# Optimization experiments

Measured on AMD Instinct MI355X. Metric: run time of the kernel, lower is better.

## Reference

```python
import jax, jax.numpy as jnp
import numpy as np

N_NODES = 50000
N_EDGES = 1600000
N_FEAT = 50
HID = 20
OUT_DIM = 10
N_GRAPHS = 64


def _glorot(key, shape):
    fan_in, fan_out = shape[0], shape[1]
    lim = float(np.sqrt(6.0 / (fan_in + fan_out)))
    return jax.random.uniform(key, shape, jnp.float32, -lim, lim)


def setup_inputs() -> dict:
    key = jax.random.key(0)
    ks = jax.random.split(key, 16)
    x = jax.random.normal(ks[0], (N_NODES, N_FEAT), jnp.float32)
    edge_index = jax.random.randint(ks[1], (2, N_EDGES), 0, N_NODES, jnp.int32)
    batch = jnp.sort(jax.random.randint(ks[2], (N_NODES,), 0, N_GRAPHS, jnp.int32))
    inp = {"x": x, "edge_index": edge_index, "batch": batch}
    # GraphConv layer params: lin_rel (weight+bias, applied to aggregated msgs), lin_root (no bias)
    dims = [(N_FEAT, HID), (HID, HID), (HID, HID)]
    for i, (di, do) in enumerate(dims, start=1):
        inp[f"W_rel{i}"] = _glorot(ks[3 * i], (di, do))
        inp[f"W_root{i}"] = _glorot(ks[3 * i + 1], (di, do))
        inp[f"b{i}"] = jnp.zeros((do,), jnp.float32)
    # final Linear on cat([max_pool, mean_pool]) -> in_features = 2*HID
    inp["W_lin"] = _glorot(ks[13], (2 * HID, OUT_DIM))
    inp["b_lin"] = jnp.zeros((OUT_DIM,), jnp.float32)
    return inp


def _graph_conv(x, src, dst, W_rel, W_root, b):
    # PyG GraphConv: aggregate raw neighbor features (sum), then linear.
    agg = jax.ops.segment_sum(x[src], dst, num_segments=N_NODES)  # [N, d_in]
    return agg @ W_rel + x @ W_root + b


def reference(x, edge_index, batch,
              W_rel1, W_root1, b1,
              W_rel2, W_root2, b2,
              W_rel3, W_root3, b3,
              W_lin, b_lin):
    src, dst = edge_index[0], edge_index[1]
    h = jax.nn.relu(_graph_conv(x, src, dst, W_rel1, W_root1, b1))
    h = jax.nn.relu(_graph_conv(h, src, dst, W_rel2, W_root2, b2))
    h = jax.nn.relu(_graph_conv(h, src, dst, W_rel3, W_root3, b3))
    # global max / mean pool per graph
    maxP = jax.ops.segment_max(h, batch, num_segments=N_GRAPHS)  # [G, HID]
    sums = jax.ops.segment_sum(h, batch, num_segments=N_GRAPHS)
    cnt = jax.ops.segment_sum(jnp.ones((h.shape[0], 1), h.dtype), batch, num_segments=N_GRAPHS)
    meanP = sums / jnp.maximum(cnt, 1.0)
    return jnp.concatenate([maxP, meanP], axis=-1) @ W_lin + b_lin
```

## Files before the change

### kernel.cpp

```cpp
#include <hip/hip_runtime.h>

#define N_NODES  50000
#define N_EDGES  1600000
#define N_FEAT   50
#define HID      20
#define OUT_DIM  10
#define N_GRAPHS 64

#define NBUCK 196
#define BCAP  10240
#define EPB   (N_EDGES/256)
#define G50B  977


__global__ __launch_bounds__(1024) void k1_gemm_scatter(
        const float* __restrict__ x, const float* __restrict__ Wrel,
        const float* __restrict__ Wroot, const float* __restrict__ b,
        float* __restrict__ y, float* __restrict__ acc,
        const int* __restrict__ dst, const int* __restrict__ srcv,
        int* __restrict__ gcur, unsigned int* __restrict__ padded,
        float* __restrict__ gmax, float* __restrict__ gsum, float* __restrict__ gcnt) {
    __shared__ char smem[55120];
    int t = threadIdx.x;
    if (blockIdx.x < G50B) {
        if (blockIdx.x == 0) {
            for (int i = t; i < N_GRAPHS * HID; i += 1024) { gmax[i] = 0.f; gsum[i] = 0.f; }
            if (t < N_GRAPHS) gcnt[t] = 0.f;
        }
        float* sWrel  = (float*)smem;
        float* sWroot = sWrel + N_FEAT * HID;
        for (int i = t; i < N_FEAT * HID; i += 1024) { sWrel[i] = Wrel[i]; sWroot[i] = Wroot[i]; }
        __syncthreads();
        int idx = blockIdx.x * 1024 + t;
        if (idx < N_NODES * HID) {
            int n = idx / HID, j = idx % HID;
            const float* xr = x + n * N_FEAT;
            float a0 = 0.f, a1 = b[j];
            #pragma unroll
            for (int k = 0; k < N_FEAT; ++k) {
                float xv = xr[k];
                a0 = fmaf(xv, sWrel[k * HID + j], a0);
                a1 = fmaf(xv, sWroot[k * HID + j], a1);
            }
            y[idx] = a0; acc[idx] = a1;
        }
    } else {
        unsigned int* ep   = (unsigned int*)smem;
        unsigned int* ep2  = ep + EPB;
        int* cnt   = (int*)(ep2 + EPB);
        int* scn   = cnt + 256;
        int* lofs  = scn + 256;
        int* gbase = lofs + 256;
        int* lcur  = gbase + 256;
        if (t < 256) cnt[t] = 0;
        __syncthreads();
        int e0 = (blockIdx.x - G50B) * EPB;
        for (int i = t; i < EPB; i += 1024) {
            int d = dst[e0 + i], s = srcv[e0 + i];
            ep[i] = ((unsigned int)d << 16) | (unsigned int)s;
            atomicAdd(&cnt[d >> 8], 1);
        }
        __syncthreads();
        if (t < 256) scn[t] = cnt[t];
        __syncthreads();
        for (int d = 1; d < 256; d <<= 1) {
            int u = 0;
            if (t < 256 && t >= d) u = scn[t - d];
            __syncthreads();
            if (t < 256) scn[t] += u;
            __syncthreads();
        }
        if (t < NBUCK) {
            int excl = scn[t] - cnt[t];
            lofs[t] = excl; lcur[t] = excl;
            gbase[t] = t * BCAP + atomicAdd(&gcur[t], cnt[t]);
        }
        __syncthreads();
        for (int i = t; i < EPB; i += 1024) {
            unsigned int e = ep[i];
            int p = atomicAdd(&lcur[e >> 24], 1);
            ep2[p] = e;
        }
        __syncthreads();
        for (int i = t; i < EPB; i += 1024) {
            unsigned int e = ep2[i];
            int bb = e >> 24;
            int gp = gbase[bb] + (i - lofs[bb]);
            if (gp < (bb + 1) * BCAP) padded[gp] = e;
        }
    }
}


__global__ __launch_bounds__(1024) void k2_build_gather(
        const int* __restrict__ gcur, const unsigned int* __restrict__ padded,
        unsigned short* __restrict__ csr16, int* __restrict__ startg,
        int* __restrict__ cntg, unsigned short* __restrict__ permg,
        const float* __restrict__ y_in, const float* __restrict__ accp,
        const float* __restrict__ Wrel, const float* __restrict__ Wroot,
        const float* __restrict__ b,
        float* __restrict__ y_out, float* __restrict__ acc_out) {
    __shared__ unsigned short eo[BCAP];
    __shared__ float rh[256 * HID];
    __shared__ float sWrel[HID * HID], sWroot[HID * HID], sb[HID];
    __shared__ int cnt4[4][256], cur4[4][256];
    __shared__ int scn[256], s_start[256], s_cnt[256];
    __shared__ unsigned short sperm[256];
    int g = blockIdx.x, t = threadIdx.x, wg = t >> 8;
    int base = g * BCAP;
    int m = min(gcur[g], BCAP);
    int n0 = g * 256, nvalid = min(256, N_NODES - n0);
    for (int i = t; i < HID * HID; i += 1024) { sWrel[i] = Wrel[i]; sWroot[i] = Wroot[i]; }
    if (t < HID) sb[t] = b[t];
    if (t < 256) { cnt4[0][t] = 0; cnt4[1][t] = 0; cnt4[2][t] = 0; cnt4[3][t] = 0; }
    for (int i = t; i < nvalid * HID; i += 1024) rh[i] = accp[n0 * HID + i];
    __syncthreads();
    for (int i = t; i < m; i += 1024)
        atomicAdd(&cnt4[wg][(padded[base + i] >> 16) & 255u], 1);
    __syncthreads();
    int c0 = 0, c1 = 0, c2 = 0, tot = 0;
    if (t < 256) {
        c0 = cnt4[0][t]; c1 = cnt4[1][t]; c2 = cnt4[2][t]; int c3 = cnt4[3][t];
        tot = c0 + c1 + c2 + c3;
        scn[t] = tot; s_cnt[t] = tot;
    }
    __syncthreads();
    for (int d = 1; d < 256; d <<= 1) {
        int u = 0;
        if (t < 256 && t >= d) u = scn[t - d];
        __syncthreads();
        if (t < 256) scn[t] += u;
        __syncthreads();
    }
    if (t < 256) {
        int excl = scn[t] - tot;
        s_start[t] = excl;
        cur4[0][t] = excl; cur4[1][t] = excl + c0;
        cur4[2][t] = excl + c0 + c1; cur4[3][t] = excl + c0 + c1 + c2;
        int node = n0 + t;
        if (node < N_NODES) { startg[node] = base + excl; cntg[node] = tot; }
    }
    __syncthreads();
    for (int i = t; i < m; i += 1024) {
        unsigned int e = padded[base + i];
        int p = atomicAdd(&cur4[wg][(e >> 16) & 255u], 1);
        eo[p] = (unsigned short)(e & 0xFFFFu);
    }
    __syncthreads();
    for (int i = t; i < m; i += 1024) csr16[base + i] = eo[i];
    if (t < 256) {
        int d = s_cnt[t], rank = 0;
        for (int j2 = 0; j2 < 256; ++j2) {
            int dj = s_cnt[j2];
            rank += (dj > d) || (dj == d && j2 < t);
        }
        sperm[rank] = (unsigned short)t;
    }
    __syncthreads();
    if (t < 256) permg[n0 + t] = sperm[t];
    int grp = t >> 3, lane = t & 7;
    if (lane < 5) {
        int q4 = lane * 4;
        #pragma unroll
        for (int rep = 0; rep < 2; ++rep) {
            int rank = rep ? 255 - grp : grp;
            int nl = sperm[rank];
            if (nl >= nvalid) continue;
            int a = s_start[nl], e = a + s_cnt[nl];
            float4 s0 = make_float4(0.f, 0.f, 0.f, 0.f);
            float4 s1 = make_float4(0.f, 0.f, 0.f, 0.f);
            int k = a;
            for (; k + 3 < e; k += 4) {
                int sn0 = eo[k], sn1 = eo[k + 1], sn2 = eo[k + 2], sn3 = eo[k + 3];
                float4 v0 = *(const float4*)(y_in + sn0 * HID + q4);
                float4 v1 = *(const float4*)(y_in + sn1 * HID + q4);
                float4 v2 = *(const float4*)(y_in + sn2 * HID + q4);
                float4 v3 = *(const float4*)(y_in + sn3 * HID + q4);
                s0.x += v0.x + v2.x; s0.y += v0.y + v2.y;
                s0.z += v0.z + v2.z; s0.w += v0.w + v2.w;
                s1.x += v1.x + v3.x; s1.y += v1.y + v3.y;
                s1.z += v1.z + v3.z; s1.w += v1.w + v3.w;
            }
            for (; k < e; ++k) {
                int sn = eo[k];
                float4 v = *(const float4*)(y_in + sn * HID + q4);
                s0.x += v.x; s0.y += v.y; s0.z += v.z; s0.w += v.w;
            }
            float* rp = &rh[nl * HID + q4];
            rp[0] += s0.x + s1.x; rp[1] += s0.y + s1.y;
            rp[2] += s0.z + s1.z; rp[3] += s0.w + s1.w;
        }
    }
    __syncthreads();
    for (int i = t; i < nvalid * 5; i += 1024) {
        int n = i / 5, j0 = (i % 5) * 4;
        float y0 = 0.f, y1 = 0.f, y2 = 0.f, y3 = 0.f;
        float a0 = sb[j0], a1 = sb[j0 + 1], a2 = sb[j0 + 2], a3 = sb[j0 + 3];
        #pragma unroll
        for (int k = 0; k < HID; ++k) {
            float h = fmaxf(rh[n * HID + k], 0.f);
            const float* wr = sWrel  + k * HID + j0;
            const float* wo = sWroot + k * HID + j0;
            y0 = fmaf(h, wr[0], y0); y1 = fmaf(h, wr[1], y1);
            y2 = fmaf(h, wr[2], y2); y3 = fmaf(h, wr[3], y3);
            a0 = fmaf(h, wo[0], a0); a1 = fmaf(h, wo[1], a1);
            a2 = fmaf(h, wo[2], a2); a3 = fmaf(h, wo[3], a3);
        }
        *(float4*)(y_out   + (n0 + n) * HID + j0) = make_float4(y0, y1, y2, y3);
        *(float4*)(acc_out + (n0 + n) * HID + j0) = make_float4(a0, a1, a2, a3);
    }
}


__global__ __launch_bounds__(1024) void k3_gather_gemm(
        const int* __restrict__ startg, const int* __restrict__ cntg,
        const unsigned short* __restrict__ csr16, const unsigned short* __restrict__ permg,
        const float* __restrict__ y_in, const float* __restrict__ accp,
        const float* __restrict__ Wrel, const float* __restrict__ Wroot,
        const float* __restrict__ b,
        float* __restrict__ y_out, float* __restrict__ acc_out) {
    __shared__ float rh[256 * HID];
    __shared__ float sWrel[HID * HID], sWroot[HID * HID], sb[HID];
    int g = blockIdx.x, t = threadIdx.x;
    int n0 = g * 256, nvalid = min(256, N_NODES - n0);
    for (int i = t; i < HID * HID; i += 1024) { sWrel[i] = Wrel[i]; sWroot[i] = Wroot[i]; }
    if (t < HID) sb[t] = b[t];
    for (int i = t; i < nvalid * HID; i += 1024) rh[i] = accp[n0 * HID + i];
    __syncthreads();
    int grp = t >> 3, lane = t & 7;
    if (lane < 5) {
        int q4 = lane * 4;
        #pragma unroll
        for (int rep = 0; rep < 2; ++rep) {
            int rank = rep ? 255 - grp : grp;
            int nl = permg[n0 + rank];
            if (nl >= nvalid) continue;
            int node = n0 + nl;
            int a = startg[node], e = a + cntg[node];
            float4 s0 = make_float4(0.f, 0.f, 0.f, 0.f);
            float4 s1 = make_float4(0.f, 0.f, 0.f, 0.f);
            int k = a;
            for (; k + 3 < e; k += 4) {
                int sn0 = csr16[k], sn1 = csr16[k + 1], sn2 = csr16[k + 2], sn3 = csr16[k + 3];
                float4 v0 = *(const float4*)(y_in + sn0 * HID + q4);
                float4 v1 = *(const float4*)(y_in + sn1 * HID + q4);
                float4 v2 = *(const float4*)(y_in + sn2 * HID + q4);
                float4 v3 = *(const float4*)(y_in + sn3 * HID + q4);
                s0.x += v0.x + v2.x; s0.y += v0.y + v2.y;
                s0.z += v0.z + v2.z; s0.w += v0.w + v2.w;
                s1.x += v1.x + v3.x; s1.y += v1.y + v3.y;
                s1.z += v1.z + v3.z; s1.w += v1.w + v3.w;
            }
            for (; k < e; ++k) {
                int sn = csr16[k];
                float4 v = *(const float4*)(y_in + sn * HID + q4);
                s0.x += v.x; s0.y += v.y; s0.z += v.z; s0.w += v.w;
            }
            float* rp = &rh[nl * HID + q4];
            rp[0] += s0.x + s1.x; rp[1] += s0.y + s1.y;
            rp[2] += s0.z + s1.z; rp[3] += s0.w + s1.w;
        }
    }
    __syncthreads();
    for (int i = t; i < nvalid * 5; i += 1024) {
        int n = i / 5, j0 = (i % 5) * 4;
        float y0 = 0.f, y1 = 0.f, y2 = 0.f, y3 = 0.f;
        float a0 = sb[j0], a1 = sb[j0 + 1], a2 = sb[j0 + 2], a3 = sb[j0 + 3];
        #pragma unroll
        for (int k = 0; k < HID; ++k) {
            float h = fmaxf(rh[n * HID + k], 0.f);
            const float* wr = sWrel  + k * HID + j0;
            const float* wo = sWroot + k * HID + j0;
            y0 = fmaf(h, wr[0], y0); y1 = fmaf(h, wr[1], y1);
            y2 = fmaf(h, wr[2], y2); y3 = fmaf(h, wr[3], y3);
            a0 = fmaf(h, wo[0], a0); a1 = fmaf(h, wo[1], a1);
            a2 = fmaf(h, wo[2], a2); a3 = fmaf(h, wo[3], a3);
        }
        *(float4*)(y_out   + (n0 + n) * HID + j0) = make_float4(y0, y1, y2, y3);
        *(float4*)(acc_out + (n0 + n) * HID + j0) = make_float4(a0, a1, a2, a3);
    }
}


__global__ __launch_bounds__(1024) void k4_gather_pool(
        const int* __restrict__ startg, const int* __restrict__ cntg,
        const unsigned short* __restrict__ csr16, const unsigned short* __restrict__ permg,
        const float* __restrict__ y_in, const float* __restrict__ accp,
        const int* __restrict__ batch,
        float* __restrict__ gmax, float* __restrict__ gsum, float* __restrict__ gcnt) {
    __shared__ float rh[256 * HID];
    __shared__ float redm[51 * HID], reds[51 * HID];
    __shared__ int sbatch[256];
    __shared__ int seglo[16], seghi[16];
    int g = blockIdx.x, t = threadIdx.x;
    int n0 = g * 256, nvalid = min(256, N_NODES - n0);
    for (int i = t; i < nvalid * HID; i += 1024) rh[i] = accp[n0 * HID + i];
    if (t < nvalid) sbatch[t] = batch[n0 + t];
    __syncthreads();
    int grp = t >> 3, lane = t & 7;
    if (lane < 5) {
        int q4 = lane * 4;
        #pragma unroll
        for (int rep = 0; rep < 2; ++rep) {
            int rank = rep ? 255 - grp : grp;
            int nl = permg[n0 + rank];
            if (nl >= nvalid) continue;
            int node = n0 + nl;
            int a = startg[node], e = a + cntg[node];
            float4 s0 = make_float4(0.f, 0.f, 0.f, 0.f);
            float4 s1 = make_float4(0.f, 0.f, 0.f, 0.f);
            int k = a;
            for (; k + 3 < e; k += 4) {
                int sn0 = csr16[k], sn1 = csr16[k + 1], sn2 = csr16[k + 2], sn3 = csr16[k + 3];
                float4 v0 = *(const float4*)(y_in + sn0 * HID + q4);
                float4 v1 = *(const float4*)(y_in + sn1 * HID + q4);
                float4 v2 = *(const float4*)(y_in + sn2 * HID + q4);
                float4 v3 = *(const float4*)(y_in + sn3 * HID + q4);
                s0.x += v0.x + v2.x; s0.y += v0.y + v2.y;
                s0.z += v0.z + v2.z; s0.w += v0.w + v2.w;
                s1.x += v1.x + v3.x; s1.y += v1.y + v3.y;
                s1.z += v1.z + v3.z; s1.w += v1.w + v3.w;
            }
            for (; k < e; ++k) {
                int sn = csr16[k];
                float4 v = *(const float4*)(y_in + sn * HID + q4);
                s0.x += v.x; s0.y += v.y; s0.z += v.z; s0.w += v.w;
            }
            float* rp = &rh[nl * HID + q4];
            rp[0] += s0.x + s1.x; rp[1] += s0.y + s1.y;
            rp[2] += s0.z + s1.z; rp[3] += s0.w + s1.w;
        }
    }
    __syncthreads();
    int g0 = sbatch[0];
    int span = sbatch[nvalid - 1] - g0 + 1;
    if (t < nvalid) {
        int bi = sbatch[t] - g0;
        if (bi < 16) {
            if (t == 0 || sbatch[t - 1] != sbatch[t]) seglo[bi] = t;
            if (t == nvalid - 1 || sbatch[t + 1] != sbatch[t]) seghi[bi] = t + 1;
        }
    }
    __syncthreads();
    if (span > 16) span = 16;
    for (int li = 0; li < span; ++li) {
        int lo = seglo[li], hi = seghi[li];
        int r = t / HID, j = t % HID;
        if (r < 51) {
            float mx = 0.f, sm = 0.f;
            for (int n = lo + r; n < hi; n += 51) {
                float v = fmaxf(rh[n * HID + j], 0.f);
                mx = fmaxf(mx, v); sm += v;
            }
            redm[r * HID + j] = mx; reds[r * HID + j] = sm;
        }
        __syncthreads();
        if (t < HID) {
            float mm = 0.f, ss = 0.f;
            #pragma unroll 17
            for (int r2 = 0; r2 < 51; ++r2) {
                mm = fmaxf(mm, redm[r2 * HID + t]);
                ss += reds[r2 * HID + t];
            }
            atomicMax((int*)&gmax[(g0 + li) * HID + t], __float_as_int(mm));
            atomicAdd(&gsum[(g0 + li) * HID + t], ss);
        }
        if (t == HID) atomicAdd(&gcnt[g0 + li], (float)(hi - lo));
        __syncthreads();
    }
}


__global__ __launch_bounds__(640) void final_lin(const float* __restrict__ gmax,
        const float* __restrict__ gsum, const float* __restrict__ gcnt,
        const float* __restrict__ Wlin, const float* __restrict__ blin,
        float* __restrict__ out) {
    __shared__ float sW[2 * HID * OUT_DIM];
    for (int i = threadIdx.x; i < 2 * HID * OUT_DIM; i += 640) sW[i] = Wlin[i];
    __syncthreads();
    int idx = threadIdx.x;
    if (idx >= N_GRAPHS * OUT_DIM) return;
    int g = idx / OUT_DIM, o = idx % OUT_DIM;
    float c = fmaxf(gcnt[g], 1.0f);
    float a = blin[o];
    #pragma unroll
    for (int j = 0; j < HID; ++j) {
        a = fmaf(gmax[g * HID + j], sW[j * OUT_DIM + o], a);
        a = fmaf(gsum[g * HID + j] / c, sW[(HID + j) * OUT_DIM + o], a);
    }
    out[idx] = a;
}

extern "C" void kernel_launch(void* const* d_in, const int* in_sizes, int n_in,
                              void* d_out, int out_size, void* d_ws, size_t ws_size,
                              hipStream_t stream) {
    const float* x      = (const float*)d_in[0];
    const int*   ei     = (const int*)  d_in[1];
    const int*   batch  = (const int*)  d_in[2];
    const float* Wrel1  = (const float*)d_in[3];
    const float* Wroot1 = (const float*)d_in[4];
    const float* b1     = (const float*)d_in[5];
    const float* Wrel2  = (const float*)d_in[6];
    const float* Wroot2 = (const float*)d_in[7];
    const float* b2     = (const float*)d_in[8];
    const float* Wrel3  = (const float*)d_in[9];
    const float* Wroot3 = (const float*)d_in[10];
    const float* b3     = (const float*)d_in[11];
    const float* Wlin   = (const float*)d_in[12];
    const float* blin   = (const float*)d_in[13];
    float* out = (float*)d_out;

    char* ws = (char*)d_ws;
    const size_t NB = (size_t)N_NODES * HID * sizeof(float);
    const size_t PB = (size_t)NBUCK * BCAP * sizeof(int);
    const size_t CB = (size_t)NBUCK * BCAP * sizeof(unsigned short);
    const size_t NP = (size_t)NBUCK * 256;
    float*          yA     = (float*)(ws);
    float*          yB     = (float*)(ws + NB);
    float*          accA   = (float*)(ws + 2 * NB);
    float*          accB   = (float*)(ws + 3 * NB);
    unsigned int*   padded = (unsigned int*)(ws + 4 * NB);
    unsigned short* csr16  = (unsigned short*)(ws + 4 * NB + PB);
    int*            startg = (int*)(ws + 4 * NB + PB + CB);
    int*            cntg   = startg + NP;
    unsigned short* permg  = (unsigned short*)(cntg + NP);
    int*            gcur   = (int*)((char*)permg + NP * sizeof(unsigned short));
    float*          gmax   = (float*)(gcur + 256);
    float*          gsum   = gmax + N_GRAPHS * HID;
    float*          gcnt   = gsum + N_GRAPHS * HID;

    const int* src = ei;
    const int* dst = ei + N_EDGES;

    hipMemsetAsync(gcur, 0, NBUCK * sizeof(int), stream);
    k1_gemm_scatter<<<G50B + 256, 1024, 0, stream>>>(x, Wrel1, Wroot1, b1, yA, accA,
                                                     dst, src, gcur, padded,
                                                     gmax, gsum, gcnt);
    k2_build_gather<<<NBUCK, 1024, 0, stream>>>(gcur, padded, csr16, startg, cntg, permg,
                                                yA, accA, Wrel2, Wroot2, b2, yB, accB);
    k3_gather_gemm<<<NBUCK, 1024, 0, stream>>>(startg, cntg, csr16, permg,
                                               yB, accB, Wrel3, Wroot3, b3, yA, accA);
    k4_gather_pool<<<NBUCK, 1024, 0, stream>>>(startg, cntg, csr16, permg,
                                               yA, accA, batch, gmax, gsum, gcnt);
    final_lin<<<1, 640, 0, stream>>>(gmax, gsum, gcnt, Wlin, blin, out);
}
```

Measured before the change: 116.8 us.

## Rebucket edges into 256 balanced buckets, pad y stride, fuse final linear

Edges are now binned into 256 buckets of about 196 nodes each, keyed by a multiply-shift hash, using per-edge shared-memory atomic ranks instead of the in-block radix reorder. The CSR build reuses those ranks so it no longer needs per-warp-group count arrays and a second atomic pass. The y feature rows are padded to a 32-float stride so gathered float4 rows stay cache-line aligned. The final linear layer is folded into the pool kernel through a last-block completion counter, which removes one launch. The scatter blocks are moved ahead of the GEMM blocks in the first kernel's grid. In exchange the padded y arrays add memory traffic and a threadfence is needed at the end of every pool block.

```diff
diff --git a/kernel.cpp b/kernel.cpp
--- a/kernel.cpp
+++ b/kernel.cpp
@@ -7,86 +7,68 @@
 #define OUT_DIM  10
 #define N_GRAPHS 64
 
-#define NBUCK 196
-#define BCAP  10240
+#define NBUCK 256
+#define BCAP  8192
 #define EPB   (N_EDGES/256)
-#define G50B  977
-
-
-__global__ __launch_bounds__(1024) void k1_gemm_scatter(
-        const float* __restrict__ x, const float* __restrict__ Wrel,
-        const float* __restrict__ Wroot, const float* __restrict__ b,
-        float* __restrict__ y, float* __restrict__ acc,
+#define YSTR  32
+#define GEMMB 977
+
+__device__ __forceinline__ int bstart(int b) { return (b * 65536 + 334) / 335; }
+
+
+__global__ __launch_bounds__(1024) void k1_scatter_gemm(
         const int* __restrict__ dst, const int* __restrict__ srcv,
         int* __restrict__ gcur, unsigned int* __restrict__ padded,
+        const float* __restrict__ x, const float* __restrict__ Wrel,
+        const float* __restrict__ Wroot, const float* __restrict__ bb,
+        float* __restrict__ y, float* __restrict__ acc,
         float* __restrict__ gmax, float* __restrict__ gsum, float* __restrict__ gcnt) {
-    __shared__ char smem[55120];
+    __shared__ char smem[14560];
     int t = threadIdx.x;
-    if (blockIdx.x < G50B) {
+    if (blockIdx.x < 256) {
+        unsigned short* rnk = (unsigned short*)smem;
+        int* cnt   = (int*)(smem + 12512);
+        int* gbase = cnt + 256;
         if (blockIdx.x == 0) {
             for (int i = t; i < N_GRAPHS * HID; i += 1024) { gmax[i] = 0.f; gsum[i] = 0.f; }
             if (t < N_GRAPHS) gcnt[t] = 0.f;
         }
+        if (t < 256) cnt[t] = 0;
+        __syncthreads();
+        int e0 = blockIdx.x * EPB;
+        for (int i = t; i < EPB; i += 1024) {
+            unsigned int d = (unsigned int)dst[e0 + i];
+            unsigned int key = (d * 335u) >> 16;
+            rnk[i] = (unsigned short)atomicAdd(&cnt[key], 1);
+        }
+        __syncthreads();
+        if (t < 256) gbase[t] = t * BCAP + atomicAdd(&gcur[t], cnt[t]);
+        __syncthreads();
+        for (int i = t; i < EPB; i += 1024) {
+            unsigned int d = (unsigned int)dst[e0 + i];
+            unsigned int s = (unsigned int)srcv[e0 + i];
+            unsigned int key = (d * 335u) >> 16;
+            int gp = gbase[key] + rnk[i];
+            if (gp < (int)(key + 1) * BCAP) padded[gp] = (d << 16) | s;
+        }
+    } else {
         float* sWrel  = (float*)smem;
         float* sWroot = sWrel + N_FEAT * HID;
         for (int i = t; i < N_FEAT * HID; i += 1024) { sWrel[i] = Wrel[i]; sWroot[i] = Wroot[i]; }
         __syncthreads();
-        int idx = blockIdx.x * 1024 + t;
+        int idx = (blockIdx.x - 256) * 1024 + t;
         if (idx < N_NODES * HID) {
             int n = idx / HID, j = idx % HID;
             const float* xr = x + n * N_FEAT;
-            float a0 = 0.f, a1 = b[j];
+            float a0 = 0.f, a1 = bb[j];
             #pragma unroll
             for (int k = 0; k < N_FEAT; ++k) {
                 float xv = xr[k];
                 a0 = fmaf(xv, sWrel[k * HID + j], a0);
                 a1 = fmaf(xv, sWroot[k * HID + j], a1);
             }
-            y[idx] = a0; acc[idx] = a1;
-        }
-    } else {
-        unsigned int* ep   = (unsigned int*)smem;
-        unsigned int* ep2  = ep + EPB;
-        int* cnt   = (int*)(ep2 + EPB);
-        int* scn   = cnt + 256;
-        int* lofs  = scn + 256;
-        int* gbase = lofs + 256;
-        int* lcur  = gbase + 256;
-        if (t < 256) cnt[t] = 0;
-        __syncthreads();
-        int e0 = (blockIdx.x - G50B) * EPB;
-        for (int i = t; i < EPB; i += 1024) {
-            int d = dst[e0 + i], s = srcv[e0 + i];
-            ep[i] = ((unsigned int)d << 16) | (unsigned int)s;
-            atomicAdd(&cnt[d >> 8], 1);
-        }
-        __syncthreads();
-        if (t < 256) scn[t] = cnt[t];
-        __syncthreads();
-        for (int d = 1; d < 256; d <<= 1) {
-            int u = 0;
-            if (t < 256 && t >= d) u = scn[t - d];
-            __syncthreads();
-            if (t < 256) scn[t] += u;
-            __syncthreads();
-        }
-        if (t < NBUCK) {
-            int excl = scn[t] - cnt[t];
-            lofs[t] = excl; lcur[t] = excl;
-            gbase[t] = t * BCAP + atomicAdd(&gcur[t], cnt[t]);
-        }
-        __syncthreads();
-        for (int i = t; i < EPB; i += 1024) {
-            unsigned int e = ep[i];
-            int p = atomicAdd(&lcur[e >> 24], 1);
-            ep2[p] = e;
-        }
-        __syncthreads();
-        for (int i = t; i < EPB; i += 1024) {
-            unsigned int e = ep2[i];
-            int bb = e >> 24;
-            int gp = gbase[bb] + (i - lofs[bb]);
-            if (gp < (bb + 1) * BCAP) padded[gp] = e;
+            y[n * YSTR + j] = a0;
+            acc[idx] = a1;
         }
     }
 }
@@ -98,32 +80,31 @@
         int* __restrict__ cntg, unsigned short* __restrict__ permg,
         const float* __restrict__ y_in, const float* __restrict__ accp,
         const float* __restrict__ Wrel, const float* __restrict__ Wroot,
-        const float* __restrict__ b,
+        const float* __restrict__ bb,
         float* __restrict__ y_out, float* __restrict__ acc_out) {
     __shared__ unsigned short eo[BCAP];
-    __shared__ float rh[256 * HID];
+    __shared__ char uni[20480];
     __shared__ float sWrel[HID * HID], sWroot[HID * HID], sb[HID];
-    __shared__ int cnt4[4][256], cur4[4][256];
-    __shared__ int scn[256], s_start[256], s_cnt[256];
+    __shared__ int cnt[256], scn[256], s_start[256], s_cnt[256];
     __shared__ unsigned short sperm[256];
-    int g = blockIdx.x, t = threadIdx.x, wg = t >> 8;
+    unsigned short* rnk = (unsigned short*)uni;
+    float*          rh  = (float*)uni;
+    int g = blockIdx.x, t = threadIdx.x;
     int base = g * BCAP;
     int m = min(gcur[g], BCAP);
-    int n0 = g * 256, nvalid = min(256, N_NODES - n0);
+    int n0 = bstart(g);
+    int n1 = min(bstart(g + 1), N_NODES);
+    int nvalid = n1 - n0;
     for (int i = t; i < HID * HID; i += 1024) { sWrel[i] = Wrel[i]; sWroot[i] = Wroot[i]; }
-    if (t < HID) sb[t] = b[t];
-    if (t < 256) { cnt4[0][t] = 0; cnt4[1][t] = 0; cnt4[2][t] = 0; cnt4[3][t] = 0; }
-    for (int i = t; i < nvalid * HID; i += 1024) rh[i] = accp[n0 * HID + i];
-    __syncthreads();
-    for (int i = t; i < m; i += 1024)
-        atomicAdd(&cnt4[wg][(padded[base + i] >> 16) & 255u], 1);
-    __syncthreads();
-    int c0 = 0, c1 = 0, c2 = 0, tot = 0;
-    if (t < 256) {
-        c0 = cnt4[0][t]; c1 = cnt4[1][t]; c2 = cnt4[2][t]; int c3 = cnt4[3][t];
-        tot = c0 + c1 + c2 + c3;
-        scn[t] = tot; s_cnt[t] = tot;
-    }
+    if (t < HID) sb[t] = bb[t];
+    if (t < 256) cnt[t] = 0;
+    __syncthreads();
+    for (int i = t; i < m; i += 1024) {
+        int local = (int)(padded[base + i] >> 16) - n0;
+        rnk[i] = (unsigned short)atomicAdd(&cnt[local], 1);
+    }
+    __syncthreads();
+    if (t < 256) { s_cnt[t] = cnt[t]; scn[t] = cnt[t]; }
     __syncthreads();
     for (int d = 1; d < 256; d <<= 1) {
         int u = 0;
@@ -133,18 +114,14 @@
         __syncthreads();
     }
     if (t < 256) {
-        int excl = scn[t] - tot;
-        s_start[t] = excl;
-        cur4[0][t] = excl; cur4[1][t] = excl + c0;
-        cur4[2][t] = excl + c0 + c1; cur4[3][t] = excl + c0 + c1 + c2;
-        int node = n0 + t;
-        if (node < N_NODES) { startg[node] = base + excl; cntg[node] = tot; }
+        s_start[t] = scn[t] - s_cnt[t];
+        if (t < nvalid) { startg[n0 + t] = base + s_start[t]; cntg[n0 + t] = s_cnt[t]; }
     }
     __syncthreads();
     for (int i = t; i < m; i += 1024) {
         unsigned int e = padded[base + i];
-        int p = atomicAdd(&cur4[wg][(e >> 16) & 255u], 1);
-        eo[p] = (unsigned short)(e & 0xFFFFu);
+        int local = (int)(e >> 16) - n0;
+        eo[s_start[local] + rnk[i]] = (unsigned short)(e & 0xFFFFu);
     }
     __syncthreads();
     for (int i = t; i < m; i += 1024) csr16[base + i] = eo[i];
@@ -157,7 +134,9 @@
         sperm[rank] = (unsigned short)t;
     }
     __syncthreads();
-    if (t < 256) permg[n0 + t] = sperm[t];
+    if (t < 256) permg[g * 256 + t] = sperm[t];
+    for (int i = t; i < nvalid * HID; i += 1024) rh[i] = accp[n0 * HID + i];
+    __syncthreads();
     int grp = t >> 3, lane = t & 7;
     if (lane < 5) {
         int q4 = lane * 4;
@@ -165,30 +144,31 @@
         for (int rep = 0; rep < 2; ++rep) {
             int rank = rep ? 255 - grp : grp;
             int nl = sperm[rank];
-            if (nl >= nvalid) continue;
-            int a = s_start[nl], e = a + s_cnt[nl];
-            float4 s0 = make_float4(0.f, 0.f, 0.f, 0.f);
-            float4 s1 = make_float4(0.f, 0.f, 0.f, 0.f);
-            int k = a;
-            for (; k + 3 < e; k += 4) {
-                int sn0 = eo[k], sn1 = eo[k + 1], sn2 = eo[k + 2], sn3 = eo[k + 3];
-                float4 v0 = *(const float4*)(y_in + sn0 * HID + q4);
-                float4 v1 = *(const float4*)(y_in + sn1 * HID + q4);
-                float4 v2 = *(const float4*)(y_in + sn2 * HID + q4);
-                float4 v3 = *(const float4*)(y_in + sn3 * HID + q4);
-                s0.x += v0.x + v2.x; s0.y += v0.y + v2.y;
-                s0.z += v0.z + v2.z; s0.w += v0.w + v2.w;
-                s1.x += v1.x + v3.x; s1.y += v1.y + v3.y;
-                s1.z += v1.z + v3.z; s1.w += v1.w + v3.w;
-            }
-            for (; k < e; ++k) {
-                int sn = eo[k];
-                float4 v = *(const float4*)(y_in + sn * HID + q4);
-                s0.x += v.x; s0.y += v.y; s0.z += v.z; s0.w += v.w;
-            }
-            float* rp = &rh[nl * HID + q4];
-            rp[0] += s0.x + s1.x; rp[1] += s0.y + s1.y;
-            rp[2] += s0.z + s1.z; rp[3] += s0.w + s1.w;
+            if (nl < nvalid) {
+                int a = s_start[nl], e = a + s_cnt[nl];
+                float4 s0 = make_float4(0.f, 0.f, 0.f, 0.f);
+                float4 s1 = make_float4(0.f, 0.f, 0.f, 0.f);
+                int k = a;
+                for (; k + 3 < e; k += 4) {
+                    int sn0 = eo[k], sn1 = eo[k + 1], sn2 = eo[k + 2], sn3 = eo[k + 3];
+                    float4 v0 = *(const float4*)(y_in + sn0 * YSTR + q4);
+                    float4 v1 = *(const float4*)(y_in + sn1 * YSTR + q4);
+                    float4 v2 = *(const float4*)(y_in + sn2 * YSTR + q4);
+                    float4 v3 = *(const float4*)(y_in + sn3 * YSTR + q4);
+                    s0.x += v0.x + v2.x; s0.y += v0.y + v2.y;
+                    s0.z += v0.z + v2.z; s0.w += v0.w + v2.w;
+                    s1.x += v1.x + v3.x; s1.y += v1.y + v3.y;
+                    s1.z += v1.z + v3.z; s1.w += v1.w + v3.w;
+                }
+                for (; k < e; ++k) {
+                    int sn = eo[k];
+                    float4 v = *(const float4*)(y_in + sn * YSTR + q4);
+                    s0.x += v.x; s0.y += v.y; s0.z += v.z; s0.w += v.w;
+                }
+                float* rp = &rh[nl * HID + q4];
+                rp[0] += s0.x + s1.x; rp[1] += s0.y + s1.y;
+                rp[2] += s0.z + s1.z; rp[3] += s0.w + s1.w;
+            }
         }
     }
     __syncthreads();
@@ -206,8 +186,8 @@
             a0 = fmaf(h, wo[0], a0); a1 = fmaf(h, wo[1], a1);
             a2 = fmaf(h, wo[2], a2); a3 = fmaf(h, wo[3], a3);
         }
-        *(float4*)(y_out   + (n0 + n) * HID + j0) = make_float4(y0, y1, y2, y3);
-        *(float4*)(acc_out + (n0 + n) * HID + j0) = make_float4(a0, a1, a2, a3);
+        *(float4*)(y_out   + (n0 + n) * YSTR + j0) = make_float4(y0, y1, y2, y3);
+        *(float4*)(acc_out + (n0 + n) * HID  + j0) = make_float4(a0, a1, a2, a3);
     }
 }
 
@@ -217,14 +197,16 @@
         const unsigned short* __restrict__ csr16, const unsigned short* __restrict__ permg,
         const float* __restrict__ y_in, const float* __restrict__ accp,
         const float* __restrict__ Wrel, const float* __restrict__ Wroot,
-        const float* __restrict__ b,
+        const float* __restrict__ bb,
         float* __restrict__ y_out, float* __restrict__ acc_out) {
     __shared__ float rh[256 * HID];
     __shared__ float sWrel[HID * HID], sWroot[HID * HID], sb[HID];
     int g = blockIdx.x, t = threadIdx.x;
-    int n0 = g * 256, nvalid = min(256, N_NODES - n0);
+    int n0 = bstart(g);
+    int n1 = min(bstart(g + 1), N_NODES);
+    int nvalid = n1 - n0;
     for (int i = t; i < HID * HID; i += 1024) { sWrel[i] = Wrel[i]; sWroot[i] = Wroot[i]; }
-    if (t < HID) sb[t] = b[t];
+    if (t < HID) sb[t] = bb[t];
     for (int i = t; i < nvalid * HID; i += 1024) rh[i] = accp[n0 * HID + i];
     __syncthreads();
     int grp = t >> 3, lane = t & 7;
@@ -233,32 +215,33 @@
         #pragma unroll
         for (int rep = 0; rep < 2; ++rep) {
             int rank = rep ? 255 - grp : grp;
-            int nl = permg[n0 + rank];
-            if (nl >= nvalid) continue;
-            int node = n0 + nl;
-            int a = startg[node], e = a + cntg[node];
-            float4 s0 = make_float4(0.f, 0.f, 0.f, 0.f);
-            float4 s1 = make_float4(0.f, 0.f, 0.f, 0.f);
-            int k = a;
-            for (; k + 3 < e; k += 4) {
-                int sn0 = csr16[k], sn1 = csr16[k + 1], sn2 = csr16[k + 2], sn3 = csr16[k + 3];
-                float4 v0 = *(const float4*)(y_in + sn0 * HID + q4);
-                float4 v1 = *(const float4*)(y_in + sn1 * HID + q4);
-                float4 v2 = *(const float4*)(y_in + sn2 * HID + q4);
-                float4 v3 = *(const float4*)(y_in + sn3 * HID + q4);
-                s0.x += v0.x + v2.x; s0.y += v0.y + v2.y;
-                s0.z += v0.z + v2.z; s0.w += v0.w + v2.w;
-                s1.x += v1.x + v3.x; s1.y += v1.y + v3.y;
-                s1.z += v1.z + v3.z; s1.w += v1.w + v3.w;
-            }
-            for (; k < e; ++k) {
-                int sn = csr16[k];
-                float4 v = *(const float4*)(y_in + sn * HID + q4);
-                s0.x += v.x; s0.y += v.y; s0.z += v.z; s0.w += v.w;
-            }
-            float* rp = &rh[nl * HID + q4];
-            rp[0] += s0.x + s1.x; rp[1] += s0.y + s1.y;
-            rp[2] += s0.z + s1.z; rp[3] += s0.w + s1.w;
+            int nl = permg[g * 256 + rank];
+            if (nl < nvalid) {
+                int node = n0 + nl;
+                int a = startg[node], e = a + cntg[node];
+                float4 s0 = make_float4(0.f, 0.f, 0.f, 0.f);
+                float4 s1 = make_float4(0.f, 0.f, 0.f, 0.f);
+                int k = a;
+                for (; k + 3 < e; k += 4) {
+                    int sn0 = csr16[k], sn1 = csr16[k + 1], sn2 = csr16[k + 2], sn3 = csr16[k + 3];
+                    float4 v0 = *(const float4*)(y_in + sn0 * YSTR + q4);
+                    float4 v1 = *(const float4*)(y_in + sn1 * YSTR + q4);
+                    float4 v2 = *(const float4*)(y_in + sn2 * YSTR + q4);
+                    float4 v3 = *(const float4*)(y_in + sn3 * YSTR + q4);
+                    s0.x += v0.x + v2.x; s0.y += v0.y + v2.y;
+                    s0.z += v0.z + v2.z; s0.w += v0.w + v2.w;
+                    s1.x += v1.x + v3.x; s1.y += v1.y + v3.y;
+                    s1.z += v1.z + v3.z; s1.w += v1.w + v3.w;
+                }
+                for (; k < e; ++k) {
+                    int sn = csr16[k];
+                    float4 v = *(const float4*)(y_in + sn * YSTR + q4);
+                    s0.x += v.x; s0.y += v.y; s0.z += v.z; s0.w += v.w;
+                }
+                float* rp = &rh[nl * HID + q4];
+                rp[0] += s0.x + s1.x; rp[1] += s0.y + s1.y;
+                rp[2] += s0.z + s1.z; rp[3] += s0.w + s1.w;
+            }
         }
     }
     __syncthreads();
@@ -276,8 +259,8 @@
             a0 = fmaf(h, wo[0], a0); a1 = fmaf(h, wo[1], a1);
             a2 = fmaf(h, wo[2], a2); a3 = fmaf(h, wo[3], a3);
         }
-        *(float4*)(y_out   + (n0 + n) * HID + j0) = make_float4(y0, y1, y2, y3);
-        *(float4*)(acc_out + (n0 + n) * HID + j0) = make_float4(a0, a1, a2, a3);
+        *(float4*)(y_out   + (n0 + n) * YSTR + j0) = make_float4(y0, y1, y2, y3);
+        *(float4*)(acc_out + (n0 + n) * HID  + j0) = make_float4(a0, a1, a2, a3);
     }
 }
 
@@ -287,13 +270,18 @@
         const unsigned short* __restrict__ csr16, const unsigned short* __restrict__ permg,
         const float* __restrict__ y_in, const float* __restrict__ accp,
         const int* __restrict__ batch,
-        float* __restrict__ gmax, float* __restrict__ gsum, float* __restrict__ gcnt) {
+        float* __restrict__ gmax, float* __restrict__ gsum, float* __restrict__ gcnt,
+        int* __restrict__ done, const float* __restrict__ Wlin,
+        const float* __restrict__ blin, float* __restrict__ out) {
     __shared__ float rh[256 * HID];
     __shared__ float redm[51 * HID], reds[51 * HID];
     __shared__ int sbatch[256];
     __shared__ int seglo[16], seghi[16];
+    __shared__ int lastFlag;
     int g = blockIdx.x, t = threadIdx.x;
-    int n0 = g * 256, nvalid = min(256, N_NODES - n0);
+    int n0 = bstart(g);
+    int n1 = min(bstart(g + 1), N_NODES);
+    int nvalid = n1 - n0;
     for (int i = t; i < nvalid * HID; i += 1024) rh[i] = accp[n0 * HID + i];
     if (t < nvalid) sbatch[t] = batch[n0 + t];
     __syncthreads();
@@ -303,32 +291,33 @@
         #pragma unroll
         for (int rep = 0; rep < 2; ++rep) {
             int rank = rep ? 255 - grp : grp;
-            int nl = permg[n0 + rank];
-            if (nl >= nvalid) continue;
-            int node = n0 + nl;
-            int a = startg[node], e = a + cntg[node];
-            float4 s0 = make_float4(0.f, 0.f, 0.f, 0.f);
-            float4 s1 = make_float4(0.f, 0.f, 0.f, 0.f);
-            int k = a;
-            for (; k + 3 < e; k += 4) {
-                int sn0 = csr16[k], sn1 = csr16[k + 1], sn2 = csr16[k + 2], sn3 = csr16[k + 3];
-                float4 v0 = *(const float4*)(y_in + sn0 * HID + q4);
-                float4 v1 = *(const float4*)(y_in + sn1 * HID + q4);
-                float4 v2 = *(const float4*)(y_in + sn2 * HID + q4);
-                float4 v3 = *(const float4*)(y_in + sn3 * HID + q4);
-                s0.x += v0.x + v2.x; s0.y += v0.y + v2.y;
-                s0.z += v0.z + v2.z; s0.w += v0.w + v2.w;
-                s1.x += v1.x + v3.x; s1.y += v1.y + v3.y;
-                s1.z += v1.z + v3.z; s1.w += v1.w + v3.w;
-            }
-            for (; k < e; ++k) {
-                int sn = csr16[k];
-                float4 v = *(const float4*)(y_in + sn * HID + q4);
-                s0.x += v.x; s0.y += v.y; s0.z += v.z; s0.w += v.w;
-            }
-            float* rp = &rh[nl * HID + q4];
-            rp[0] += s0.x + s1.x; rp[1] += s0.y + s1.y;
-            rp[2] += s0.z + s1.z; rp[3] += s0.w + s1.w;
+            int nl = permg[g * 256 + rank];
+            if (nl < nvalid) {
+                int node = n0 + nl;
+                int a = startg[node], e = a + cntg[node];
+                float4 s0 = make_float4(0.f, 0.f, 0.f, 0.f);
+                float4 s1 = make_float4(0.f, 0.f, 0.f, 0.f);
+                int k = a;
+                for (; k + 3 < e; k += 4) {
+                    int sn0 = csr16[k], sn1 = csr16[k + 1], sn2 = csr16[k + 2], sn3 = csr16[k + 3];
+                    float4 v0 = *(const float4*)(y_in + sn0 * YSTR + q4);
+                    float4 v1 = *(const float4*)(y_in + sn1 * YSTR + q4);
+                    float4 v2 = *(const float4*)(y_in + sn2 * YSTR + q4);
+                    float4 v3 = *(const float4*)(y_in + sn3 * YSTR + q4);
+                    s0.x += v0.x + v2.x; s0.y += v0.y + v2.y;
+                    s0.z += v0.z + v2.z; s0.w += v0.w + v2.w;
+                    s1.x += v1.x + v3.x; s1.y += v1.y + v3.y;
+                    s1.z += v1.z + v3.z; s1.w += v1.w + v3.w;
+                }
+                for (; k < e; ++k) {
+                    int sn = csr16[k];
+                    float4 v = *(const float4*)(y_in + sn * YSTR + q4);
+                    s0.x += v.x; s0.y += v.y; s0.z += v.z; s0.w += v.w;
+                }
+                float* rp = &rh[nl * HID + q4];
+                rp[0] += s0.x + s1.x; rp[1] += s0.y + s1.y;
+                rp[2] += s0.z + s1.z; rp[3] += s0.w + s1.w;
+            }
         }
     }
     __syncthreads();
@@ -368,27 +357,27 @@
         if (t == HID) atomicAdd(&gcnt[g0 + li], (float)(hi - lo));
         __syncthreads();
     }
-}
-
-
-__global__ __launch_bounds__(640) void final_lin(const float* __restrict__ gmax,
-        const float* __restrict__ gsum, const float* __restrict__ gcnt,
-        const float* __restrict__ Wlin, const float* __restrict__ blin,
-        float* __restrict__ out) {
-    __shared__ float sW[2 * HID * OUT_DIM];
-    for (int i = threadIdx.x; i < 2 * HID * OUT_DIM; i += 640) sW[i] = Wlin[i];
-    __syncthreads();
-    int idx = threadIdx.x;
-    if (idx >= N_GRAPHS * OUT_DIM) return;
-    int g = idx / OUT_DIM, o = idx % OUT_DIM;
-    float c = fmaxf(gcnt[g], 1.0f);
-    float a = blin[o];
-    #pragma unroll
-    for (int j = 0; j < HID; ++j) {
-        a = fmaf(gmax[g * HID + j], sW[j * OUT_DIM + o], a);
-        a = fmaf(gsum[g * HID + j] / c, sW[(HID + j) * OUT_DIM + o], a);
-    }
-    out[idx] = a;
+    if (t == 0) {
+        __threadfence();
+        lastFlag = (atomicAdd(done, 1) == NBUCK - 1);
+    }
+    __syncthreads();
+    if (!lastFlag) return;
+    __threadfence();
+    float* sW = redm;
+    for (int i = t; i < 2 * HID * OUT_DIM; i += 1024) sW[i] = Wlin[i];
+    __syncthreads();
+    if (t < N_GRAPHS * OUT_DIM) {
+        int gg = t / OUT_DIM, o = t % OUT_DIM;
+        float c = fmaxf(gcnt[gg], 1.0f);
+        float a = blin[o];
+        #pragma unroll
+        for (int j = 0; j < HID; ++j) {
+            a = fmaf(gmax[gg * HID + j], sW[j * OUT_DIM + o], a);
+            a = fmaf(gsum[gg * HID + j] / c, sW[(HID + j) * OUT_DIM + o], a);
+        }
+        out[t] = a;
+    }
 }
 
 extern "C" void kernel_launch(void* const* d_in, const int* in_sizes, int n_in,
@@ -411,36 +400,37 @@
     float* out = (float*)d_out;
 
     char* ws = (char*)d_ws;
-    const size_t NB = (size_t)N_NODES * HID * sizeof(float);
+    const size_t YB = (size_t)N_NODES * YSTR * sizeof(float);
+    const size_t AB = (size_t)N_NODES * HID * sizeof(float);
     const size_t PB = (size_t)NBUCK * BCAP * sizeof(int);
     const size_t CB = (size_t)NBUCK * BCAP * sizeof(unsigned short);
-    const size_t NP = (size_t)NBUCK * 256;
     float*          yA     = (float*)(ws);
-    float*          yB     = (float*)(ws + NB);
-    float*          accA   = (float*)(ws + 2 * NB);
-    float*          accB   = (float*)(ws + 3 * NB);
-    unsigned int*   padded = (unsigned int*)(ws + 4 * NB);
-    unsigned short* csr16  = (unsigned short*)(ws + 4 * NB + PB);
-    int*            startg = (int*)(ws + 4 * NB + PB + CB);
-    int*            cntg   = startg + NP;
-    unsigned short* permg  = (unsigned short*)(cntg + NP);
-    int*            gcur   = (int*)((char*)permg + NP * sizeof(unsigned short));
-    float*          gmax   = (float*)(gcur + 256);
+    float*          yB     = (float*)(ws + YB);
+    float*          accA   = (float*)(ws + 2 * YB);
+    float*          accB   = (float*)(ws + 2 * YB + AB);
+    unsigned int*   padded = (unsigned int*)(ws + 2 * YB + 2 * AB);
+    unsigned short* csr16  = (unsigned short*)(ws + 2 * YB + 2 * AB + PB);
+    int*            startg = (int*)(ws + 2 * YB + 2 * AB + PB + CB);
+    int*            cntg   = startg + N_NODES;
+    unsigned short* permg  = (unsigned short*)(cntg + N_NODES);
+    int*            gcur   = (int*)((char*)permg + (size_t)NBUCK * 256 * 2);
+    int*            done   = gcur + NBUCK;
+    float*          gmax   = (float*)(done + 4);
     float*          gsum   = gmax + N_GRAPHS * HID;
     float*          gcnt   = gsum + N_GRAPHS * HID;
 
     const int* src = ei;
     const int* dst = ei + N_EDGES;
 
-    hipMemsetAsync(gcur, 0, NBUCK * sizeof(int), stream);
-    k1_gemm_scatter<<<G50B + 256, 1024, 0, stream>>>(x, Wrel1, Wroot1, b1, yA, accA,
-                                                     dst, src, gcur, padded,
-                                                     gmax, gsum, gcnt);
+    hipMemsetAsync(gcur, 0, (NBUCK + 1) * sizeof(int), stream);
+    k1_scatter_gemm<<<256 + GEMMB, 1024, 0, stream>>>(dst, src, gcur, padded,
+                                                      x, Wrel1, Wroot1, b1, yA, accA,
+                                                      gmax, gsum, gcnt);
     k2_build_gather<<<NBUCK, 1024, 0, stream>>>(gcur, padded, csr16, startg, cntg, permg,
                                                 yA, accA, Wrel2, Wroot2, b2, yB, accB);
     k3_gather_gemm<<<NBUCK, 1024, 0, stream>>>(startg, cntg, csr16, permg,
                                                yB, accB, Wrel3, Wroot3, b3, yA, accA);
     k4_gather_pool<<<NBUCK, 1024, 0, stream>>>(startg, cntg, csr16, permg,
-                                               yA, accA, batch, gmax, gsum, gcnt);
-    final_lin<<<1, 640, 0, stream>>>(gmax, gsum, gcnt, Wlin, blin, out);
+                                               yA, accA, batch, gmax, gsum, gcnt,
+                                               done, Wlin, blin, out);
 }
```

Measured after the change: 122.3 us. 4.7% more time.
